# Performance work log

Hardware: AMD Instinct MI355X
Metric: run time of the kernel (lower is better)

Reference implementation:

```python
import jax, jax.numpy as jnp
import numpy as np
from jax import lax

B, C_IN, H, W = 32, 128, 64, 64
E = 384           # embed_dim
EB = E // 3       # per-branch channels
RED = 16          # ChannelAttention reduction -> hidden 384//16 = 24


def _conv(x, w, b, k):
    # x: [B,C,H,W], w: [O,I,k,k] (OIHW), 'same' padding k//2, stride 1
    p = k // 2
    y = lax.conv_general_dilated(x, w, (1, 1), [(p, p), (p, p)],
                                 dimension_numbers=('NCHW', 'OIHW', 'NCHW'))
    return y + b[None, :, None, None]


def setup_inputs() -> dict:
    key = jax.random.key(0)
    ks = jax.random.split(key, 8)

    def he(k, shape, fan_k, cout):
        fan_out = fan_k * fan_k * cout
        return jax.random.normal(k, shape, jnp.float32) * np.sqrt(2.0 / fan_out)

    x = jax.random.normal(ks[0], (B, C_IN, H, W), jnp.float32)
    w3 = he(ks[1], (EB, C_IN, 3, 3), 3, EB)
    w5 = he(ks[2], (EB, C_IN, 5, 5), 5, EB)
    w7 = he(ks[3], (EB, C_IN, 7, 7), 7, EB)
    ca_w1 = jax.random.normal(ks[4], (E // RED, E), jnp.float32) * 0.02
    ca_w2 = jax.random.normal(ks[5], (E, E // RED), jnp.float32) * 0.02
    fusion_w = he(ks[6], (E, E), 1, E)
    return {
        'x': x,
        'w3': w3, 'b3': jnp.zeros((EB,), jnp.float32),
        'w5': w5, 'b5': jnp.zeros((EB,), jnp.float32),
        'w7': w7, 'b7': jnp.zeros((EB,), jnp.float32),
        'ca_w1': ca_w1, 'ca_w2': ca_w2,
        'fusion_w': fusion_w, 'fusion_b': jnp.zeros((E,), jnp.float32),
        'ln_g': jnp.ones((E,), jnp.float32), 'ln_b': jnp.zeros((E,), jnp.float32),
    }


def reference(x, w3, b3, w5, b5, w7, b7, ca_w1, ca_w2, fusion_w, fusion_b, ln_g, ln_b):
    # multi-scale conv branches (strides all 1 -> identical HxW, no interpolation needed)
    f3 = _conv(x, w3, b3, 3)
    f5 = _conv(x, w5, b5, 5)
    f7 = _conv(x, w7, b7, 7)
    fused = jnp.concatenate([f3, f5, f7], axis=1)        # [B, E, H, W]

    # ChannelAttention (CBAM-style): shared MLP over global avg & max pool, sigmoid gate
    avg = jnp.mean(fused, axis=(2, 3))                   # [B, E]
    mx = jnp.max(fused, axis=(2, 3))                     # [B, E]
    def mlp(v):
        return jax.nn.relu(v @ ca_w1.T) @ ca_w2.T
    attn = jax.nn.sigmoid(mlp(avg) + mlp(mx))            # [B, E]
    fused = fused * attn[:, :, None, None]

    # 1x1 fusion conv
    fused = jnp.einsum('bchw,oc->bohw', fused, fusion_w) + fusion_b[None, :, None, None]

    # flatten to tokens + LayerNorm
    Bb, Ee, Hh, Ww = fused.shape
    t = fused.reshape(Bb, Ee, Hh * Ww).transpose(0, 2, 1)  # [B, N, E]
    mu = jnp.mean(t, axis=-1, keepdims=True)
    var = jnp.var(t, axis=-1, keepdims=True)
    t = (t - mu) / jnp.sqrt(var + 1e-5) * ln_g + ln_b
    return t
```

## Files before the change

kernel.cpp:

```cpp
#include <hip/hip_runtime.h>

#define BB 32
#define CIN 128
#define HH 64
#define WW 64
#define EE 384
#define EBC 128
#define HID 24
#define NPIX (HH*WW)
#define NTOK (BB*NPIX)

#define XW 70
#define XH 72

typedef __attribute__((ext_vector_type(8))) short short8;
typedef __attribute__((ext_vector_type(4))) float f32x4;
typedef __attribute__((ext_vector_type(4))) unsigned short us4;

__device__ __forceinline__ unsigned short f2bf(float f) {
    unsigned u = __float_as_uint(f);
    unsigned r = u + 0x7fffu + ((u >> 16) & 1u);
    return (unsigned short)(r >> 16);
}
__device__ __forceinline__ float bf2f(unsigned short u) {
    return __uint_as_float(((unsigned)u) << 16);
}
__device__ __forceinline__ unsigned fmapu(float f) {
    unsigned u = __float_as_uint(f);
    return (u & 0x80000000u) ? ~u : (u | 0x80000000u);
}
__device__ __forceinline__ float funmap(unsigned u) {
    unsigned b = (u & 0x80000000u) ? (u ^ 0x80000000u) : ~u;
    return __uint_as_float(b);
}

__global__ void repack_x(const float* __restrict__ x, unsigned short* __restrict__ xh) {
    int py = blockIdx.x, b = blockIdx.y;
    int y = py - 3;
    unsigned short* orow = xh + ((size_t)(b * XH + py)) * XW * CIN;
    if ((unsigned)y >= (unsigned)HH) {
        for (int i = threadIdx.x; i < XW * CIN / 8; i += 256)
            ((short8*)orow)[i] = (short8){};
        return;
    }
    __shared__ unsigned short t[CIN][WW + 6];
    const float* xp = x + (((size_t)b * CIN) * HH + y) * WW;
    #pragma unroll
    for (int it = 0; it < 32; ++it) {
        int xc = threadIdx.x & 63;
        int c = (threadIdx.x >> 6) + it * 4;
        t[c][xc] = f2bf(xp[(size_t)c * NPIX + xc]);
    }
    __syncthreads();
    unsigned short* op = orow + 3 * CIN;
    #pragma unroll
    for (int it = 0; it < 8; ++it) {
        int id = threadIdx.x + it * 256;
        int xc = id >> 5, c0 = (id & 31) * 4;
        us4 v = { t[c0][xc], t[c0 + 1][xc], t[c0 + 2][xc], t[c0 + 3][xc] };
        *(us4*)(op + xc * CIN + c0) = v;
    }
    if (threadIdx.x < 96) {
        int pxsel = threadIdx.x >> 4;
        int px = pxsel < 3 ? pxsel : 64 + pxsel;
        ((short8*)(orow + px * CIN))[threadIdx.x & 15] = (short8){};
    }
}

__global__ void repack_w(const float* __restrict__ w3, const float* __restrict__ w5,
                         const float* __restrict__ w7, const float* __restrict__ fw,
                         unsigned short* __restrict__ wrep, unsigned short* __restrict__ fwb,
                         float* __restrict__ psum, unsigned* __restrict__ pmax) {
    int idx = blockIdx.x * 256 + threadIdx.x;
    if (idx < 83 * 16384) {
        int j = idx & 7;
        int lane = (idx >> 3) & 63;
        int mt = (idx >> 9) & 7;
        int cb = (idx >> 12) & 3;
        int t = idx >> 14;
        int l16 = lane & 15, g4 = lane >> 4;
        int o = mt * 16 + l16;
        int c = cb * 32 + g4 * 8 + j;
        float v;
        if (t < 9)       { int tt = t;      int dy = tt / 3, dx = tt % 3; v = w3[((o * CIN + c) * 3 + dy) * 3 + dx]; }
        else if (t < 34) { int tt = t - 9;  int dy = tt / 5, dx = tt % 5; v = w5[((o * CIN + c) * 5 + dy) * 5 + dx]; }
        else             { int tt = t - 34; int dy = tt / 7, dx = tt % 7; v = w7[((o * CIN + c) * 7 + dy) * 7 + dx]; }
        wrep[idx] = f2bf(v);
    }
    if (idx < EE * EE) {
        int j = idx & 7;
        int lane = (idx >> 3) & 63;
        int mc = idx >> 9;
        int m = mc % 24, cb = mc / 24;
        int l16 = lane & 15, g4 = lane >> 4;
        int o = m * 16 + l16;
        int c = cb * 32 + g4 * 8 + j;
        fwb[idx] = f2bf(fw[o * EE + c]);
    }
    if (idx < BB * EE) { psum[idx] = 0.f; pmax[idx] = 0u; }
}


#define SMEM_CHUNKS 2832

template <int KS>
__device__ __forceinline__ void conv_branch(
        const unsigned short* __restrict__ xb,
        const short8* __restrict__ wv8,
        const float* __restrict__ bias, unsigned short* __restrict__ fused,
        float* __restrict__ psum, unsigned* __restrict__ pmax,
        int b, int y0, int choff, short8* smem) {
    constexpr int PK = KS / 2;
    constexpr int RT = 4 + 2 * PK;
    constexpr int TPX = 64 + 2 * PK;
    constexpr int NCH = RT * 4 * TPX;
    constexpr int NT = KS * KS;
    constexpr int NINSTR = (NCH + 63) / 64;

    int lane = threadIdx.x & 63, wv = threadIdx.x >> 6;
    int l16 = lane & 15, g4 = lane >> 4;

    f32x4 acc[8][4];
    #pragma unroll
    for (int i = 0; i < 8; ++i)
        #pragma unroll
        for (int j = 0; j < 4; ++j) acc[i][j] = (f32x4){0.f, 0.f, 0.f, 0.f};

    for (int cb = 0; cb < 4; ++cb) {
        if (cb) __syncthreads();
        for (int k = wv; k < NINSTR; k += 4) {
            int c = k * 64 + lane;
            int rg = c / TPX;
            int p = c - rg * TPX;
            int r = rg >> 2;
            int g = rg & 3;
            const unsigned short* src = xb +
                ((size_t)((y0 + r - PK + 3) * XW + (p - PK + 3))) * CIN + cb * 32 + g * 8;
            short8* dst = smem + k * 64;
            __builtin_amdgcn_global_load_lds(
                (const __attribute__((address_space(1))) void*)src,
                (__attribute__((address_space(3))) void*)dst, 16, 0, 0);
        }
        short8 a0[8], a1[8];
        {
            const short8* wf = wv8 + ((size_t)(cb * 8)) * 64 + lane;
            #pragma unroll
            for (int mt = 0; mt < 8; ++mt) a0[mt] = wf[mt * 64];
        }
        __syncthreads();

        #pragma unroll
        for (int t = 0; t < NT; ++t) {
            short8* ac = (t & 1) ? a1 : a0;
            short8* an = (t & 1) ? a0 : a1;
            int dy = t / KS, dx = t % KS;
            int lrow = ((wv + dy) * 4 + g4) * TPX + l16 + dx;
            short8 bfv[4];
            #pragma unroll
            for (int nt = 0; nt < 4; ++nt) bfv[nt] = smem[lrow + nt * 16];
            if (t + 1 < NT) {
                const short8* wf = wv8 + ((size_t)(((t + 1) * 4 + cb) * 8)) * 64 + lane;
                #pragma unroll
                for (int mt = 0; mt < 8; ++mt) an[mt] = wf[mt * 64];
            }
            __builtin_amdgcn_sched_barrier(0);
            #pragma unroll
            for (int nt = 0; nt < 4; ++nt)
                #pragma unroll
                for (int mt = 0; mt < 8; ++mt)
                    acc[mt][nt] = __builtin_amdgcn_mfma_f32_16x16x32_bf16(ac[mt], bfv[nt], acc[mt][nt], 0, 0, 0);
        }
    }

    int y = y0 + wv;
    #pragma unroll
    for (int mt = 0; mt < 8; ++mt) {
        int orow = mt * 16 + g4 * 4;
        f32x4 bv = *(const f32x4*)(bias + orow);
        float sacc[4] = {0.f, 0.f, 0.f, 0.f};
        float macc[4] = {-1e30f, -1e30f, -1e30f, -1e30f};
        #pragma unroll
        for (int nt = 0; nt < 4; ++nt) {
            int pix = y * WW + nt * 16 + l16;
            us4 pk;
            #pragma unroll
            for (int r = 0; r < 4; ++r) {
                float vv = acc[mt][nt][r] + bv[r];
                sacc[r] += vv;
                macc[r] = fmaxf(macc[r], vv);
                pk[r] = f2bf(vv);
            }
            *(us4*)(fused + ((size_t)(b * NPIX + pix)) * EE + choff + orow) = pk;
        }
        #pragma unroll
        for (int r = 0; r < 4; ++r) {
            float s = sacc[r], m = macc[r];
            #pragma unroll
            for (int sh = 1; sh < 16; sh <<= 1) {
                s += __shfl_xor(s, sh);
                m = fmaxf(m, __shfl_xor(m, sh));
            }
            if (l16 == 0) {
                atomicAdd(&psum[b * EE + choff + orow + r], s);
                atomicMax(&pmax[b * EE + choff + orow + r], fmapu(m));
            }
        }
    }
}

__global__ __launch_bounds__(256, 2) void conv_all(
        const unsigned short* __restrict__ xh, const unsigned short* __restrict__ wrep,
        const float* __restrict__ b3, const float* __restrict__ b5, const float* __restrict__ b7,
        unsigned short* __restrict__ fused, float* __restrict__ psum, unsigned* __restrict__ pmax) {
    __shared__ short8 smem[SMEM_CHUNKS];
    int z = blockIdx.z;
    int br = z % 3;
    int b = z / 3;
    int y0 = blockIdx.x * 4;
    const unsigned short* xb = xh + (size_t)b * (XH * XW * CIN);
    if (br == 0)
        conv_branch<7>(xb, (const short8*)(wrep + 34 * 16384), b7, fused, psum, pmax, b, y0, 256, smem);
    else if (br == 1)
        conv_branch<5>(xb, (const short8*)(wrep + 9 * 16384),  b5, fused, psum, pmax, b, y0, 128, smem);
    else
        conv_branch<3>(xb, (const short8*)(wrep + 0 * 16384),  b3, fused, psum, pmax, b, y0, 0, smem);
}

__global__ void attn_kernel(const float* __restrict__ psum, const unsigned* __restrict__ pmax,
                            const float* __restrict__ ca_w1, const float* __restrict__ ca_w2,
                            float* __restrict__ attn) {
    int b = blockIdx.x;
    __shared__ float av[EE], mxv[EE], hsum[HID];
    int t = threadIdx.x;
    if (t < EE) {
        av[t] = psum[b * EE + t] * (1.0f / (float)NPIX);
        mxv[t] = funmap(pmax[b * EE + t]);
    }
    __syncthreads();
    if (t < HID) {
        float sa = 0.f, sm = 0.f;
        for (int c = 0; c < EE; ++c) {
            float w = ca_w1[t * EE + c];
            sa += w * av[c];
            sm += w * mxv[c];
        }
        hsum[t] = fmaxf(sa, 0.f) + fmaxf(sm, 0.f);
    }
    __syncthreads();
    if (t < EE) {
        float s = 0.f;
        for (int h = 0; h < HID; ++h) s += ca_w2[t * HID + h] * hsum[h];
        attn[b * EE + t] = 1.f / (1.f + __expf(-s));
    }
}

#define BPITCH 392
__global__ __launch_bounds__(256, 2) void fuse_ln(
        const unsigned short* __restrict__ fused, const unsigned short* __restrict__ fwb,
        const float* __restrict__ attn,
        const float* __restrict__ fusion_b, const float* __restrict__ ln_g,
        const float* __restrict__ ln_b, float* __restrict__ out) {
    int b = blockIdx.y;
    int p0 = blockIdx.x * 64;
    int lane = threadIdx.x & 63, wv = threadIdx.x >> 6;
    int l16 = lane & 15, g4 = lane >> 4;

    __shared__ unsigned short sB[64 * BPITCH];
    __shared__ float sattn[EE];
    __shared__ float s_sum[4][64], s_sq[4][64], s_mean[64], s_rstd[64];

    for (int i = threadIdx.x; i < EE; i += 256) sattn[i] = attn[b * EE + i];
    __syncthreads();

    const unsigned short* fb = fused + ((size_t)(b * NPIX + p0)) * EE;
    for (int i = threadIdx.x; i < 64 * 48; i += 256) {
        int cg = i % 48, tok = i / 48;
        short8 raw = *(const short8*)(fb + tok * EE + cg * 8);
        short8 o;
        #pragma unroll
        for (int j = 0; j < 8; ++j)
            o[j] = (short)f2bf(bf2f((unsigned short)raw[j]) * sattn[cg * 8 + j]);
        *(short8*)(sB + tok * BPITCH + cg * 8) = o;
    }
    __syncthreads();

    f32x4 acc[6][4];
    #pragma unroll
    for (int i = 0; i < 6; ++i)
        #pragma unroll
        for (int j = 0; j < 4; ++j) acc[i][j] = (f32x4){0.f, 0.f, 0.f, 0.f};

    const short8* fw8 = (const short8*)fwb;
    for (int cb = 0; cb < 12; ++cb) {
        int c0 = cb * 32 + g4 * 8;
        short8 a[6];
        #pragma unroll
        for (int mt = 0; mt < 6; ++mt)
            a[mt] = fw8[(cb * 24 + wv * 6 + mt) * 64 + lane];
        #pragma unroll
        for (int nt = 0; nt < 4; ++nt) {
            short8 bf = *(const short8*)(sB + (nt * 16 + l16) * BPITCH + c0);
            #pragma unroll
            for (int mt = 0; mt < 6; ++mt)
                acc[mt][nt] = __builtin_amdgcn_mfma_f32_16x16x32_bf16(a[mt], bf, acc[mt][nt], 0, 0, 0);
        }
    }

    #pragma unroll
    for (int nt = 0; nt < 4; ++nt) {
        float ps = 0.f, pq = 0.f;
        #pragma unroll
        for (int mt = 0; mt < 6; ++mt) {
            int o = wv * 96 + mt * 16 + g4 * 4;
            f32x4 bv = *(const f32x4*)(fusion_b + o);
            #pragma unroll
            for (int r = 0; r < 4; ++r) {
                float v = acc[mt][nt][r] + bv[r];
                acc[mt][nt][r] = v;
                ps += v;
                pq += v * v;
            }
        }
        ps += __shfl_xor(ps, 16); pq += __shfl_xor(pq, 16);
        ps += __shfl_xor(ps, 32); pq += __shfl_xor(pq, 32);
        if (g4 == 0) { s_sum[wv][nt * 16 + l16] = ps; s_sq[wv][nt * 16 + l16] = pq; }
    }
    __syncthreads();
    if (threadIdx.x < 64) {
        int pix = threadIdx.x;
        float s = 0.f, q = 0.f;
        #pragma unroll
        for (int w = 0; w < 4; ++w) { s += s_sum[w][pix]; q += s_sq[w][pix]; }
        float mean = s * (1.0f / (float)EE);
        float var = q * (1.0f / (float)EE) - mean * mean;
        s_mean[pix] = mean;
        s_rstd[pix] = rsqrtf(var + 1e-5f);
    }
    __syncthreads();

    #pragma unroll
    for (int nt = 0; nt < 4; ++nt) {
        int pix = nt * 16 + l16;
        float mean = s_mean[pix], rstd = s_rstd[pix];
        size_t tokbase = ((size_t)(b * NPIX + p0 + pix)) * EE;
        #pragma unroll
        for (int mt = 0; mt < 6; ++mt) {
            int o = wv * 96 + mt * 16 + g4 * 4;
            f32x4 g = *(const f32x4*)(ln_g + o);
            f32x4 be = *(const f32x4*)(ln_b + o);
            f32x4 res;
            #pragma unroll
            for (int r = 0; r < 4; ++r)
                res[r] = (acc[mt][nt][r] - mean) * rstd * g[r] + be[r];
            *(f32x4*)(out + tokbase + o) = res;
        }
    }
}

extern "C" void kernel_launch(void* const* d_in, const int* in_sizes, int n_in,
                              void* d_out, int out_size, void* d_ws, size_t ws_size,
                              hipStream_t stream) {
    const float* x    = (const float*)d_in[0];
    const float* w3   = (const float*)d_in[1];
    const float* b3   = (const float*)d_in[2];
    const float* w5   = (const float*)d_in[3];
    const float* b5   = (const float*)d_in[4];
    const float* w7   = (const float*)d_in[5];
    const float* b7   = (const float*)d_in[6];
    const float* caw1 = (const float*)d_in[7];
    const float* caw2 = (const float*)d_in[8];
    const float* fw   = (const float*)d_in[9];
    const float* fbias= (const float*)d_in[10];
    const float* lng  = (const float*)d_in[11];
    const float* lnb  = (const float*)d_in[12];
    float* out = (float*)d_out;

    char* ws = (char*)d_ws;
    size_t off = 0;
    unsigned short* xh   = (unsigned short*)(ws + off); off += (size_t)BB * XH * XW * CIN * 2;
    unsigned short* wrep = (unsigned short*)(ws + off); off += (size_t)83 * EBC * CIN * 2;
    unsigned short* fwb  = (unsigned short*)(ws + off); off += (size_t)EE * EE * 2;
    unsigned short* fused= (unsigned short*)(ws + off); off += (size_t)NTOK * EE * 2;
    float*    psum = (float*)(ws + off);    off += (size_t)BB * EE * 4;
    unsigned* pmax = (unsigned*)(ws + off); off += (size_t)BB * EE * 4;
    float*    attn = (float*)(ws + off);    off += (size_t)BB * EE * 4;

    repack_x<<<dim3(XH, BB), 256, 0, stream>>>(x, xh);
    repack_w<<<dim3(5312), 256, 0, stream>>>(w3, w5, w7, fw, wrep, fwb, psum, pmax);

    conv_all<<<dim3(16, 1, 3 * BB), 256, 0, stream>>>(xh, wrep, b3, b5, b7, fused, psum, pmax);

    attn_kernel<<<dim3(BB), 384, 0, stream>>>(psum, pmax, caw1, caw2, attn);
    fuse_ln<<<dim3(NPIX / 64, BB), 256, 0, stream>>>(fused, fwb, attn, fbias, lng, lnb, out);
}
```

Measured before the change: 689.2 us.

## Switch conv to 32x32x16 MFMA with 8 waves splitting output channels

```diff
diff --git a/kernel.cpp b/kernel.cpp
--- a/kernel.cpp
+++ b/kernel.cpp
@@ -15,6 +15,7 @@
 
 typedef __attribute__((ext_vector_type(8))) short short8;
 typedef __attribute__((ext_vector_type(4))) float f32x4;
+typedef __attribute__((ext_vector_type(16))) float f32x16;
 typedef __attribute__((ext_vector_type(4))) unsigned short us4;
 
 __device__ __forceinline__ unsigned short f2bf(float f) {
@@ -75,12 +76,11 @@
     if (idx < 83 * 16384) {
         int j = idx & 7;
         int lane = (idx >> 3) & 63;
-        int mt = (idx >> 9) & 7;
-        int cb = (idx >> 12) & 3;
+        int mt = (idx >> 9) & 3;
+        int kc = (idx >> 11) & 7;
         int t = idx >> 14;
-        int l16 = lane & 15, g4 = lane >> 4;
-        int o = mt * 16 + l16;
-        int c = cb * 32 + g4 * 8 + j;
+        int o = mt * 32 + (lane & 31);
+        int c = kc * 16 + (lane >> 5) * 8 + j;
         float v;
         if (t < 9)       { int tt = t;      int dy = tt / 3, dx = tt % 3; v = w3[((o * CIN + c) * 3 + dy) * 3 + dx]; }
         else if (t < 34) { int tt = t - 9;  int dy = tt / 5, dx = tt % 5; v = w5[((o * CIN + c) * 5 + dy) * 5 + dx]; }
@@ -118,17 +118,22 @@
     constexpr int NINSTR = (NCH + 63) / 64;
 
     int lane = threadIdx.x & 63, wv = threadIdx.x >> 6;
-    int l16 = lane & 15, g4 = lane >> 4;
-
-    f32x4 acc[8][4];
-    #pragma unroll
-    for (int i = 0; i < 8; ++i)
-        #pragma unroll
-        for (int j = 0; j < 4; ++j) acc[i][j] = (f32x4){0.f, 0.f, 0.f, 0.f};
-
+    int l31 = lane & 31, hi = lane >> 5;
+    int mh = wv >> 2;
+    int wrow = wv & 3;
+
+    f32x16 acc[2][2];
+    #pragma unroll
+    for (int i = 0; i < 2; ++i)
+        #pragma unroll
+        for (int j = 0; j < 2; ++j)
+            #pragma unroll
+            for (int r = 0; r < 16; ++r) acc[i][j][r] = 0.f;
+
+    #pragma unroll 1
     for (int cb = 0; cb < 4; ++cb) {
         if (cb) __syncthreads();
-        for (int k = wv; k < NINSTR; k += 4) {
+        for (int k = wv; k < NINSTR; k += 8) {
             int c = k * 64 + lane;
             int rg = c / TPX;
             int p = c - rg * TPX;
@@ -141,74 +146,74 @@
                 (const __attribute__((address_space(1))) void*)src,
                 (__attribute__((address_space(3))) void*)dst, 16, 0, 0);
         }
-        short8 a0[8], a1[8];
-        {
-            const short8* wf = wv8 + ((size_t)(cb * 8)) * 64 + lane;
-            #pragma unroll
-            for (int mt = 0; mt < 8; ++mt) a0[mt] = wf[mt * 64];
-        }
         __syncthreads();
 
         #pragma unroll
         for (int t = 0; t < NT; ++t) {
-            short8* ac = (t & 1) ? a1 : a0;
-            short8* an = (t & 1) ? a0 : a1;
             int dy = t / KS, dx = t % KS;
-            int lrow = ((wv + dy) * 4 + g4) * TPX + l16 + dx;
-            short8 bfv[4];
-            #pragma unroll
-            for (int nt = 0; nt < 4; ++nt) bfv[nt] = smem[lrow + nt * 16];
-            if (t + 1 < NT) {
-                const short8* wf = wv8 + ((size_t)(((t + 1) * 4 + cb) * 8)) * 64 + lane;
+            short8 a[2][2], bf[2][2];
+            #pragma unroll
+            for (int kc = 0; kc < 2; ++kc) {
+                const short8* wf = wv8 +
+                    ((size_t)(((t * 8 + cb * 2 + kc) * 4) + mh * 2)) * 64 + lane;
+                a[0][kc] = wf[0];
+                a[1][kc] = wf[64];
                 #pragma unroll
-                for (int mt = 0; mt < 8; ++mt) an[mt] = wf[mt * 64];
+                for (int n2 = 0; n2 < 2; ++n2)
+                    bf[n2][kc] = smem[((wrow + dy) * 4 + kc * 2 + hi) * TPX + n2 * 32 + l31 + dx];
             }
-            __builtin_amdgcn_sched_barrier(0);
-            #pragma unroll
-            for (int nt = 0; nt < 4; ++nt)
+            #pragma unroll
+            for (int kc = 0; kc < 2; ++kc)
                 #pragma unroll
-                for (int mt = 0; mt < 8; ++mt)
-                    acc[mt][nt] = __builtin_amdgcn_mfma_f32_16x16x32_bf16(ac[mt], bfv[nt], acc[mt][nt], 0, 0, 0);
-        }
-    }
-
-    int y = y0 + wv;
-    #pragma unroll
-    for (int mt = 0; mt < 8; ++mt) {
-        int orow = mt * 16 + g4 * 4;
-        f32x4 bv = *(const f32x4*)(bias + orow);
-        float sacc[4] = {0.f, 0.f, 0.f, 0.f};
-        float macc[4] = {-1e30f, -1e30f, -1e30f, -1e30f};
-        #pragma unroll
-        for (int nt = 0; nt < 4; ++nt) {
-            int pix = y * WW + nt * 16 + l16;
-            us4 pk;
+                for (int n2 = 0; n2 < 2; ++n2)
+                    #pragma unroll
+                    for (int m2 = 0; m2 < 2; ++m2)
+                        acc[m2][n2] = __builtin_amdgcn_mfma_f32_32x32x16_bf16(
+                            a[m2][kc], bf[n2][kc], acc[m2][n2], 0, 0, 0);
+        }
+    }
+
+    int y = y0 + wrow;
+    #pragma unroll
+    for (int m2 = 0; m2 < 2; ++m2) {
+        int chb = mh * 64 + m2 * 32;
+        #pragma unroll
+        for (int r4 = 0; r4 < 4; ++r4) {
+            int cho = chb + r4 * 8 + hi * 4;
+            f32x4 bv = *(const f32x4*)(bias + cho);
+            float sacc[4] = {0.f, 0.f, 0.f, 0.f};
+            float macc[4] = {-1e30f, -1e30f, -1e30f, -1e30f};
+            #pragma unroll
+            for (int n2 = 0; n2 < 2; ++n2) {
+                int pix = y * WW + n2 * 32 + l31;
+                us4 pk;
+                #pragma unroll
+                for (int r = 0; r < 4; ++r) {
+                    float vv = acc[m2][n2][r4 * 4 + r] + bv[r];
+                    sacc[r] += vv;
+                    macc[r] = fmaxf(macc[r], vv);
+                    pk[r] = f2bf(vv);
+                }
+                *(us4*)(fused + ((size_t)(b * NPIX + pix)) * EE + choff + cho) = pk;
+            }
             #pragma unroll
             for (int r = 0; r < 4; ++r) {
-                float vv = acc[mt][nt][r] + bv[r];
-                sacc[r] += vv;
-                macc[r] = fmaxf(macc[r], vv);
-                pk[r] = f2bf(vv);
+                float s = sacc[r], m = macc[r];
+                #pragma unroll
+                for (int sh = 1; sh < 32; sh <<= 1) {
+                    s += __shfl_xor(s, sh);
+                    m = fmaxf(m, __shfl_xor(m, sh));
+                }
+                if (l31 == 0) {
+                    atomicAdd(&psum[b * EE + choff + cho + r], s);
+                    atomicMax(&pmax[b * EE + choff + cho + r], fmapu(m));
+                }
             }
-            *(us4*)(fused + ((size_t)(b * NPIX + pix)) * EE + choff + orow) = pk;
-        }
-        #pragma unroll
-        for (int r = 0; r < 4; ++r) {
-            float s = sacc[r], m = macc[r];
-            #pragma unroll
-            for (int sh = 1; sh < 16; sh <<= 1) {
-                s += __shfl_xor(s, sh);
-                m = fmaxf(m, __shfl_xor(m, sh));
-            }
-            if (l16 == 0) {
-                atomicAdd(&psum[b * EE + choff + orow + r], s);
-                atomicMax(&pmax[b * EE + choff + orow + r], fmapu(m));
-            }
-        }
-    }
-}
-
-__global__ __launch_bounds__(256, 2) void conv_all(
+        }
+    }
+}
+
+__global__ __launch_bounds__(512, 4) void conv_all(
         const unsigned short* __restrict__ xh, const unsigned short* __restrict__ wrep,
         const float* __restrict__ b3, const float* __restrict__ b5, const float* __restrict__ b7,
         unsigned short* __restrict__ fused, float* __restrict__ psum, unsigned* __restrict__ pmax) {
@@ -388,7 +393,7 @@
     repack_x<<<dim3(XH, BB), 256, 0, stream>>>(x, xh);
     repack_w<<<dim3(5312), 256, 0, stream>>>(w3, w5, w7, fw, wrep, fwb, psum, pmax);
 
-    conv_all<<<dim3(16, 1, 3 * BB), 256, 0, stream>>>(xh, wrep, b3, b5, b7, fused, psum, pmax);
+    conv_all<<<dim3(16, 1, 3 * BB), 512, 0, stream>>>(xh, wrep, b3, b5, b7, fused, psum, pmax);
 
     attn_kernel<<<dim3(BB), 384, 0, stream>>>(psum, pmax, caw1, caw2, attn);
     fuse_ln<<<dim3(NPIX / 64, BB), 256, 0, stream>>>(fused, fwb, attn, fbias, lng, lnb, out);
```

New measurement: 813.9 us. 18.1% more time.
